# Kernel optimization log

Hardware: AMD Instinct MI355X
Metric: run time of the kernel (lower is better)

## Reference

```python
import jax, jax.numpy as jnp
import numpy as np

D_MODEL = 1024
NUM_HEADS = 16
HEAD_DIM = D_MODEL // NUM_HEADS


def setup_inputs() -> dict:
    key = jax.random.key(0)
    k_x, k_qw, k_qb, k_ow, k_ob = jax.random.split(key, 5)
    s = 1.0 / np.sqrt(D_MODEL)
    return {
        "x": jax.random.normal(k_x, (2, 2048, D_MODEL), dtype=jnp.float32),
        "qkv_w": jax.random.uniform(k_qw, (3 * D_MODEL, D_MODEL), jnp.float32, -s, s),
        "qkv_b": jax.random.uniform(k_qb, (3 * D_MODEL,), jnp.float32, -s, s),
        "out_w": jax.random.uniform(k_ow, (D_MODEL, D_MODEL), jnp.float32, -s, s),
        "out_b": jax.random.uniform(k_ob, (D_MODEL,), jnp.float32, -s, s),
    }


def reference(x, qkv_w, qkv_b, out_w, out_b):
    B, S, D = x.shape
    # fused QKV projection: [B,S,3D]
    qkv = jnp.einsum("bsd,ed->bse", x, qkv_w) + qkv_b
    # [B,S,H,3*hd] -> [B,H,S,3*hd]
    qkv = qkv.reshape(B, S, NUM_HEADS, 3 * HEAD_DIM).transpose(0, 2, 1, 3)
    q, k, v = jnp.split(qkv, 3, axis=-1)
    scale = 1.0 / jnp.sqrt(jnp.asarray(HEAD_DIM, x.dtype))
    scores = jnp.einsum("bhqd,bhkd->bhqk", q, k) * scale
    attn = jax.nn.softmax(scores, axis=-1)
    vals = jnp.einsum("bhqk,bhkd->bhqd", attn, v)
    vals = vals.transpose(0, 2, 1, 3).reshape(B, S, D)
    return jnp.einsum("bsd,ed->bse", vals, out_w) + out_b
```

## Files before the change

kernel.cpp:

```cpp
#include <hip/hip_runtime.h>
#include <stdint.h>


#define D_MODEL 1024
#define NUM_HEADS 16
#define HEAD_DIM 64
#define BATCH 2
#define SEQ 2048
#define M_TOT (BATCH * SEQ)
#define QKV_N (3 * D_MODEL)

typedef __attribute__((ext_vector_type(8))) short bf16x8;
typedef __attribute__((ext_vector_type(4))) short bf16x4;
typedef __attribute__((ext_vector_type(4))) float f32x4;
typedef __attribute__((ext_vector_type(4))) unsigned int u32x4;

__device__ __forceinline__ unsigned short f2bf(float f) {
    union { float f; unsigned int u; } v; v.f = f;
    unsigned int u = v.u;
    u += 0x7fffu + ((u >> 16) & 1u);
    return (unsigned short)(u >> 16);
}

__device__ __forceinline__ unsigned int exp2_bf16u(float x) {
    return (unsigned int)__builtin_fmaf(x, 128.0f, 16251.58f);
}

__device__ __forceinline__ unsigned int perm_pack(unsigned int hi, unsigned int lo) {
#if __has_builtin(__builtin_amdgcn_perm)
    return __builtin_amdgcn_perm(hi, lo, 0x05040100u);
#else
    return (lo & 0xFFFFu) | (hi << 16);
#endif
}

__device__ __forceinline__ void gld_lds16(const unsigned short* g,
                                          unsigned short* l) {
#if __has_builtin(__builtin_amdgcn_global_load_lds)
    __builtin_amdgcn_global_load_lds(
        (const __attribute__((address_space(1))) unsigned int*)g,
        (__attribute__((address_space(3))) unsigned int*)l, 16, 0, 0);
#else
    *(u32x4*)(l + (threadIdx.x & 63) * 8) = *(const u32x4*)g;
#endif
}

__global__ __launch_bounds__(256) void cvt_all(const float* __restrict__ x,
                                               const float* __restrict__ qw,
                                               const float* __restrict__ ow,
                                               unsigned short* __restrict__ xb,
                                               unsigned short* __restrict__ wqb,
                                               unsigned short* __restrict__ wob) {
    int i = blockIdx.x * 256 + threadIdx.x;
    const int N1 = M_TOT * D_MODEL / 8;
    const int N2 = N1 + QKV_N * D_MODEL / 8;
    const float* src; unsigned short* dst; int j;
    if (i < N1)      { src = x;  dst = xb;  j = i; }
    else if (i < N2) { src = qw; dst = wqb; j = i - N1; }
    else             { src = ow; dst = wob; j = i - N2; }
    const float4* s = (const float4*)src;
    float4 a = s[2 * j], b = s[2 * j + 1];
    u32x4 o;
    o.x = (unsigned int)f2bf(a.x) | ((unsigned int)f2bf(a.y) << 16);
    o.y = (unsigned int)f2bf(a.z) | ((unsigned int)f2bf(a.w) << 16);
    o.z = (unsigned int)f2bf(b.x) | ((unsigned int)f2bf(b.y) << 16);
    o.w = (unsigned int)f2bf(b.z) | ((unsigned int)f2bf(b.w) << 16);
    *(u32x4*)(dst + 8 * (size_t)j) = o;
}

__device__ __forceinline__ void gemm_tile(const unsigned short* __restrict__ A,
                                          const unsigned short* __restrict__ Bw,
                                          int K, int m0, int n0,
                                          unsigned short* As, unsigned short* Bs,
                                          f32x4 acc[4][4]) {
    const int tid = threadIdx.x;
    const int lane = tid & 63;
    const int wave = tid >> 6;
    const int wm = (wave >> 1) * 64;
    const int wn = (wave & 1) * 64;
    const int quad = lane >> 4;
    const int l16 = lane & 15;
    const int lrow = lane >> 3;
    const int sw = (lane & 7) ^ (lrow & 7);
    const int l7 = l16 & 7;

#pragma unroll
    for (int mt = 0; mt < 4; mt++)
#pragma unroll
        for (int nt = 0; nt < 4; nt++) acc[mt][nt] = (f32x4)0.0f;

    for (int kt = 0; kt < K; kt += 64) {
#pragma unroll
        for (int i = 0; i < 4; ++i) {
            int R = wave * 32 + i * 8;
            int grow = R + lrow;
            gld_lds16(A + (size_t)(m0 + grow) * K + kt + sw * 8, As + R * 64);
            gld_lds16(Bw + (size_t)(n0 + grow) * K + kt + sw * 8, Bs + R * 64);
        }
        __syncthreads();
#pragma unroll
        for (int ks = 0; ks < 2; ++ks) {
            int cxl = ((ks * 4 + quad) ^ l7) * 8;
            bf16x8 af[4], bf[4];
#pragma unroll
            for (int mt = 0; mt < 4; mt++)
                af[mt] = *(const bf16x8*)(As + (wm + mt * 16 + l16) * 64 + cxl);
#pragma unroll
            for (int nt = 0; nt < 4; nt++)
                bf[nt] = *(const bf16x8*)(Bs + (wn + nt * 16 + l16) * 64 + cxl);
#pragma unroll
            for (int mt = 0; mt < 4; mt++)
#pragma unroll
                for (int nt = 0; nt < 4; nt++)
                    acc[mt][nt] = __builtin_amdgcn_mfma_f32_16x16x32_bf16(
                        af[mt], bf[nt], acc[mt][nt], 0, 0, 0);
        }
        __syncthreads();
    }
}

__global__ __launch_bounds__(256) void gemm_qkv(const unsigned short* __restrict__ xb,
                                                const unsigned short* __restrict__ wb,
                                                const float* __restrict__ bias,
                                                unsigned short* __restrict__ qb,
                                                unsigned short* __restrict__ kb,
                                                unsigned short* __restrict__ vtb) {
    __shared__ __align__(16) unsigned short As[128 * 64];
    __shared__ __align__(16) unsigned short Bs[128 * 64];
    f32x4 acc[4][4];
    const int m0 = blockIdx.y * 128, n0 = blockIdx.x * 128;
    gemm_tile(xb, wb, D_MODEL, m0, n0, As, Bs, acc);

    const int tid = threadIdx.x;
    const int lane = tid & 63, wave = tid >> 6;
    const int wm = (wave >> 1) * 64, wn = (wave & 1) * 64;
    const int quad = lane >> 4, l16 = lane & 15;
    const float QSCALE = 0.18033688011112042f;

    const int s64 = (n0 + wn) >> 6;
    const int h = s64 / 3;
    const int sec = s64 - h * 3;
    const int bh = (m0 >> 11) * NUM_HEADS + h;
    const int sbase = (m0 + wm) & 2047;

    unsigned short* sm = ((wave & 2) ? Bs : As) + (wave & 1) * 4096;

    if (sec < 2) {
        const float scl = (sec == 0) ? QSCALE : 1.0f;
#pragma unroll
        for (int nt = 0; nt < 4; nt++) {
            int c = nt * 16 + l16;
            float bia = bias[n0 + wn + c];
#pragma unroll
            for (int mt = 0; mt < 4; mt++)
#pragma unroll
                for (int r = 0; r < 4; r++) {
                    int row = mt * 16 + quad * 4 + r;
                    sm[row * 64 + ((((c >> 3) ^ (row & 7)) << 3) | (c & 7))] =
                        f2bf((acc[mt][nt][r] + bia) * scl);
                }
        }
        unsigned short* dstb = (sec == 0) ? qb : kb;
#pragma unroll
        for (int p = 0; p < 8; p++) {
            int row = p * 8 + (lane >> 3);
            int g = lane & 7;
            u32x4 ch = *(const u32x4*)(sm + row * 64 + ((g ^ (row & 7)) << 3));
            *(u32x4*)(dstb + ((size_t)bh * SEQ + sbase + row) * 64 + g * 8) = ch;
        }
    } else {
#pragma unroll
        for (int nt = 0; nt < 4; nt++) {
            int d = nt * 16 + l16;
            float bia = bias[n0 + wn + d];
#pragma unroll
            for (int mt = 0; mt < 4; mt++) {
                int c = mt * 16 + quad * 4;
                unsigned short t4[4];
#pragma unroll
                for (int r = 0; r < 4; r++) t4[r] = f2bf(acc[mt][nt][r] + bia);
                *(uint64_t*)(sm + d * 64 +
                             ((((c >> 3) ^ (d & 7)) << 3) | (c & 7))) =
                    *(const uint64_t*)t4;
            }
        }
#pragma unroll
        for (int p = 0; p < 8; p++) {
            int row = p * 8 + (lane >> 3);
            int g = lane & 7;
            u32x4 ch = *(const u32x4*)(sm + row * 64 + ((g ^ (row & 7)) << 3));
            *(u32x4*)(vtb + ((size_t)bh * 64 + row) * SEQ + sbase + g * 8) = ch;
        }
    }
}

__global__ __launch_bounds__(256) void attn(const unsigned short* __restrict__ qb,
                                            const unsigned short* __restrict__ kb,
                                            const unsigned short* __restrict__ vtb,
                                            unsigned short* __restrict__ vals) {
    __shared__ __align__(16) unsigned short Ks[2][2][64 * 64];
    __shared__ __align__(16) unsigned short VTs[2][2][64 * 64];

    const int tid = threadIdx.x;
    const int lane = tid & 63, wave = tid >> 6;
    const int quad = lane >> 4, l16 = lane & 15;
    const int l7 = l16 & 7;
    const int bh = blockIdx.x;
    const int q0 = blockIdx.y * 128;
    const unsigned short* qh = qb + (size_t)bh * SEQ * 64;
    const unsigned short* kh = kb + (size_t)bh * SEQ * 64;
    const unsigned short* vth = vtb + (size_t)bh * 64 * SEQ;
    const int wrow = wave * 32;

    bf16x8 aq[2][2];
#pragma unroll
    for (int nq = 0; nq < 2; nq++)
#pragma unroll
        for (int ks = 0; ks < 2; ++ks)
            aq[nq][ks] = *(const bf16x8*)(
                qh + (size_t)(q0 + wrow + nq * 16 + l16) * 64 + ks * 32 + quad * 8);

    const int lrow = lane >> 3;
    const int sw = (lane & 7) ^ (lrow & 7);

    int cxl0 = ((0 * 4 + quad) ^ l7) * 8;
    int cxl1 = ((1 * 4 + quad) ^ l7) * 8;

    auto stage = [&](int t, int b) {
        int kt = t * 128;
#pragma unroll
        for (int h = 0; h < 2; ++h) {
            int kth = kt + h * 64;
#pragma unroll
            for (int i = 0; i < 2; ++i) {
                int R = wave * 16 + i * 8;
                int row = R + lrow;
                int krow = (row & 0x23) | ((row & 0x0C) << 1) | ((row & 0x10) >> 2);
                gld_lds16(kh + (size_t)(kth + krow) * 64 + sw * 8,
                          &Ks[b][h][R * 64]);
                gld_lds16(vth + (size_t)row * SEQ + kth + sw * 8,
                          &VTs[b][h][R * 64]);
            }
        }
    };

    stage(0, 0);
    __syncthreads();

    f32x4 oacc[2][4];
    f32x4 lsum[2];
#pragma unroll
    for (int mt = 0; mt < 2; mt++) {
        lsum[mt] = (f32x4)0.0f;
#pragma unroll
        for (int nt = 0; nt < 4; nt++) oacc[mt][nt] = (f32x4)0.0f;
    }

    bf16x8 ones8;
#pragma unroll
    for (int j = 0; j < 8; j++) ones8[j] = (short)0x3F80;

    const int NR = SEQ / 128;
    for (int t = 0; t < NR; ++t) {
        const int cur = t & 1;
        if (t + 1 < NR) stage(t + 1, cur ^ 1);

#pragma unroll
        for (int hf = 0; hf < 2; ++hf) {
            const unsigned short* Kc = Ks[cur][hf];
            const unsigned short* Vc = VTs[cur][hf];

            f32x4 sacc[4][2];
#pragma unroll
            for (int mk = 0; mk < 4; mk++)
#pragma unroll
                for (int nq = 0; nq < 2; nq++) sacc[mk][nq] = (f32x4)0.0f;
#pragma unroll
            for (int ks = 0; ks < 2; ++ks) {
                int cxl = ks ? cxl1 : cxl0;
                bf16x8 bk[4];
#pragma unroll
                for (int mk = 0; mk < 4; mk++)
                    bk[mk] = *(const bf16x8*)(Kc + (mk * 16 + l16) * 64 + cxl);
#pragma unroll
                for (int mk = 0; mk < 4; mk++)
#pragma unroll
                    for (int nq = 0; nq < 2; nq++)
                        sacc[mk][nq] = __builtin_amdgcn_mfma_f32_16x16x32_bf16(
                            bk[mk], aq[nq][ks], sacc[mk][nq], 0, 0, 0);
            }

            bf16x4 pf[4][2];
#pragma unroll
            for (int mk = 0; mk < 4; mk++)
#pragma unroll
                for (int nq = 0; nq < 2; nq++) {
                    unsigned int u0 = exp2_bf16u(sacc[mk][nq][0]);
                    unsigned int u1 = exp2_bf16u(sacc[mk][nq][1]);
                    unsigned int u2 = exp2_bf16u(sacc[mk][nq][2]);
                    unsigned int u3 = exp2_bf16u(sacc[mk][nq][3]);
                    union { unsigned int u[2]; bf16x4 b; } cv;
                    cv.u[0] = perm_pack(u1, u0);
                    cv.u[1] = perm_pack(u3, u2);
                    pf[mk][nq] = cv.b;
                }

#pragma unroll
            for (int w = 0; w < 2; ++w) {
                bf16x8 ap0 = __builtin_shufflevector(
                    pf[2 * w][0], pf[2 * w + 1][0], 0, 1, 2, 3, 4, 5, 6, 7);
                bf16x8 ap1 = __builtin_shufflevector(
                    pf[2 * w][1], pf[2 * w + 1][1], 0, 1, 2, 3, 4, 5, 6, 7);
                int cxl = w ? cxl1 : cxl0;
#pragma unroll
                for (int nt = 0; nt < 4; nt++) {
                    bf16x8 bv = *(const bf16x8*)(Vc + (nt * 16 + l16) * 64 + cxl);
                    oacc[0][nt] = __builtin_amdgcn_mfma_f32_16x16x32_bf16(
                        ap0, bv, oacc[0][nt], 0, 0, 0);
                    oacc[1][nt] = __builtin_amdgcn_mfma_f32_16x16x32_bf16(
                        ap1, bv, oacc[1][nt], 0, 0, 0);
                }
                lsum[0] = __builtin_amdgcn_mfma_f32_16x16x32_bf16(
                    ap0, ones8, lsum[0], 0, 0, 0);
                lsum[1] = __builtin_amdgcn_mfma_f32_16x16x32_bf16(
                    ap1, ones8, lsum[1], 0, 0, 0);
            }
        }
        __syncthreads();
    }

    const int b = bh >> 4, h = bh & 15;
#pragma unroll
    for (int mt = 0; mt < 2; mt++) {
        f32x4 inv;
#pragma unroll
        for (int r = 0; r < 4; r++) inv[r] = 1.0f / lsum[mt][r];
#pragma unroll
        for (int nt = 0; nt < 4; nt++) {
            int d = nt * 16 + l16;
#pragma unroll
            for (int r = 0; r < 4; r++) {
                int row = wrow + mt * 16 + quad * 4 + r;
                float v = oacc[mt][nt][r] * inv[r];
                vals[((size_t)(b * SEQ + q0 + row)) * D_MODEL + h * 64 + d] =
                    f2bf(v);
            }
        }
    }
}

__global__ __launch_bounds__(256) void gemm_out(const unsigned short* __restrict__ vb,
                                                const unsigned short* __restrict__ wb,
                                                const float* __restrict__ bias,
                                                float* __restrict__ out) {
    __shared__ __align__(16) unsigned short As[128 * 64];
    __shared__ __align__(16) unsigned short Bs[64 * 64];
    const int tid = threadIdx.x;
    const int lane = tid & 63, wave = tid >> 6;
    const int wm = (wave >> 1) * 64, wn = (wave & 1) * 32;
    const int quad = lane >> 4, l16 = lane & 15;
    const int lrow = lane >> 3;
    const int sw = (lane & 7) ^ (lrow & 7);
    const int l7 = l16 & 7;
    const int m0 = blockIdx.y * 128, n0 = blockIdx.x * 64;

    f32x4 acc[4][2];
#pragma unroll
    for (int mt = 0; mt < 4; mt++)
#pragma unroll
        for (int nt = 0; nt < 2; nt++) acc[mt][nt] = (f32x4)0.0f;

    for (int kt = 0; kt < D_MODEL; kt += 64) {
#pragma unroll
        for (int i = 0; i < 4; ++i) {
            int R = wave * 32 + i * 8;
            gld_lds16(vb + (size_t)(m0 + R + lrow) * D_MODEL + kt + sw * 8,
                      As + R * 64);
        }
#pragma unroll
        for (int i = 0; i < 2; ++i) {
            int R = wave * 16 + i * 8;
            gld_lds16(wb + (size_t)(n0 + R + lrow) * D_MODEL + kt + sw * 8,
                      Bs + R * 64);
        }
        __syncthreads();
#pragma unroll
        for (int ks = 0; ks < 2; ++ks) {
            int cxl = ((ks * 4 + quad) ^ l7) * 8;
            bf16x8 af[4], bf[2];
#pragma unroll
            for (int mt = 0; mt < 4; mt++)
                af[mt] = *(const bf16x8*)(As + (wm + mt * 16 + l16) * 64 + cxl);
#pragma unroll
            for (int nt = 0; nt < 2; nt++)
                bf[nt] = *(const bf16x8*)(Bs + (wn + nt * 16 + l16) * 64 + cxl);
#pragma unroll
            for (int mt = 0; mt < 4; mt++)
#pragma unroll
                for (int nt = 0; nt < 2; nt++)
                    acc[mt][nt] = __builtin_amdgcn_mfma_f32_16x16x32_bf16(
                        af[mt], bf[nt], acc[mt][nt], 0, 0, 0);
        }
        __syncthreads();
    }

#pragma unroll
    for (int mt = 0; mt < 4; mt++)
#pragma unroll
        for (int nt = 0; nt < 2; nt++) {
            int n = n0 + wn + nt * 16 + l16;
            float bia = bias[n];
#pragma unroll
            for (int r = 0; r < 4; r++) {
                int m = m0 + wm + mt * 16 + quad * 4 + r;
                out[(size_t)m * D_MODEL + n] = acc[mt][nt][r] + bia;
            }
        }
}

extern "C" void kernel_launch(void* const* d_in, const int* in_sizes, int n_in,
                              void* d_out, int out_size, void* d_ws, size_t ws_size,
                              hipStream_t stream) {
    const float* x = (const float*)d_in[0];
    const float* qkv_w = (const float*)d_in[1];
    const float* qkv_b = (const float*)d_in[2];
    const float* out_w = (const float*)d_in[3];
    const float* out_b = (const float*)d_in[4];
    float* out = (float*)d_out;

    char* ws = (char*)d_ws;
    size_t off = 0;
    auto carve = [&](size_t bytes) -> void* {
        void* p = ws + off;
        off += (bytes + 255) & ~(size_t)255;
        return p;
    };
    unsigned short* xb  = (unsigned short*)carve((size_t)M_TOT * D_MODEL * 2);
    unsigned short* wqb = (unsigned short*)carve((size_t)QKV_N * D_MODEL * 2);
    unsigned short* wob = (unsigned short*)carve((size_t)D_MODEL * D_MODEL * 2);
    unsigned short* qbuf = (unsigned short*)carve((size_t)M_TOT * D_MODEL * 2);
    unsigned short* kbuf = (unsigned short*)carve((size_t)M_TOT * D_MODEL * 2);
    unsigned short* vtb  = (unsigned short*)carve((size_t)M_TOT * D_MODEL * 2);
    unsigned short* vals = xb;

    const int NCHUNK = (M_TOT + QKV_N + D_MODEL) * D_MODEL / 8;
    cvt_all<<<NCHUNK / 256, 256, 0, stream>>>(x, qkv_w, out_w, xb, wqb, wob);

    gemm_qkv<<<dim3(QKV_N / 128, M_TOT / 128), 256, 0, stream>>>(
        xb, wqb, qkv_b, qbuf, kbuf, vtb);

    attn<<<dim3(BATCH * NUM_HEADS, SEQ / 128), 256, 0, stream>>>(
        qbuf, kbuf, vtb, vals);

    gemm_out<<<dim3(D_MODEL / 64, M_TOT / 128), 256, 0, stream>>>(
        vals, wob, out_b, out);
}
```

Baseline: 179.6 us.

## Double-buffer LDS tiles in QKV and output GEMMs to overlap loads with MFMA

Both projection GEMMs get two LDS buffers per operand. The next K-tile is issued with global-to-LDS loads into the alternate buffer while MFMAs consume the current one, which is meant to hide global-load latency behind compute. LDS use per block doubles, which may lower occupancy. Whether the async loads actually overlap depends on how gld_lds16 waits are placed relative to the remaining __syncthreads in the loop.

```diff
diff --git a/kernel.cpp b/kernel.cpp
--- a/kernel.cpp
+++ b/kernel.cpp
@@ -71,7 +71,8 @@
 __device__ __forceinline__ void gemm_tile(const unsigned short* __restrict__ A,
                                           const unsigned short* __restrict__ Bw,
                                           int K, int m0, int n0,
-                                          unsigned short* As, unsigned short* Bs,
+                                          unsigned short (*As)[128 * 64],
+                                          unsigned short (*Bs)[128 * 64],
                                           f32x4 acc[4][4]) {
     const int tid = threadIdx.x;
     const int lane = tid & 63;
@@ -89,25 +90,33 @@
 #pragma unroll
         for (int nt = 0; nt < 4; nt++) acc[mt][nt] = (f32x4)0.0f;
 
-    for (int kt = 0; kt < K; kt += 64) {
+    auto stage = [&](int kt, int b) {
 #pragma unroll
         for (int i = 0; i < 4; ++i) {
             int R = wave * 32 + i * 8;
             int grow = R + lrow;
-            gld_lds16(A + (size_t)(m0 + grow) * K + kt + sw * 8, As + R * 64);
-            gld_lds16(Bw + (size_t)(n0 + grow) * K + kt + sw * 8, Bs + R * 64);
-        }
-        __syncthreads();
+            gld_lds16(A + (size_t)(m0 + grow) * K + kt + sw * 8, As[b] + R * 64);
+            gld_lds16(Bw + (size_t)(n0 + grow) * K + kt + sw * 8, Bs[b] + R * 64);
+        }
+    };
+
+    stage(0, 0);
+    __syncthreads();
+
+    const int NT = K / 64;
+    for (int t = 0; t < NT; ++t) {
+        const int cur = t & 1;
+        if (t + 1 < NT) stage((t + 1) * 64, cur ^ 1);
 #pragma unroll
         for (int ks = 0; ks < 2; ++ks) {
             int cxl = ((ks * 4 + quad) ^ l7) * 8;
             bf16x8 af[4], bf[4];
 #pragma unroll
             for (int mt = 0; mt < 4; mt++)
-                af[mt] = *(const bf16x8*)(As + (wm + mt * 16 + l16) * 64 + cxl);
+                af[mt] = *(const bf16x8*)(As[cur] + (wm + mt * 16 + l16) * 64 + cxl);
 #pragma unroll
             for (int nt = 0; nt < 4; nt++)
-                bf[nt] = *(const bf16x8*)(Bs + (wn + nt * 16 + l16) * 64 + cxl);
+                bf[nt] = *(const bf16x8*)(Bs[cur] + (wn + nt * 16 + l16) * 64 + cxl);
 #pragma unroll
             for (int mt = 0; mt < 4; mt++)
 #pragma unroll
@@ -125,8 +134,8 @@
                                                 unsigned short* __restrict__ qb,
                                                 unsigned short* __restrict__ kb,
                                                 unsigned short* __restrict__ vtb) {
-    __shared__ __align__(16) unsigned short As[128 * 64];
-    __shared__ __align__(16) unsigned short Bs[128 * 64];
+    __shared__ __align__(16) unsigned short As[2][128 * 64];
+    __shared__ __align__(16) unsigned short Bs[2][128 * 64];
     f32x4 acc[4][4];
     const int m0 = blockIdx.y * 128, n0 = blockIdx.x * 128;
     gemm_tile(xb, wb, D_MODEL, m0, n0, As, Bs, acc);
@@ -143,7 +152,7 @@
     const int bh = (m0 >> 11) * NUM_HEADS + h;
     const int sbase = (m0 + wm) & 2047;
 
-    unsigned short* sm = ((wave & 2) ? Bs : As) + (wave & 1) * 4096;
+    unsigned short* sm = ((wave & 2) ? Bs[0] : As[0]) + (wave & 1) * 4096;
 
     if (sec < 2) {
         const float scl = (sec == 0) ? QSCALE : 1.0f;
@@ -353,8 +362,8 @@
                                                 const unsigned short* __restrict__ wb,
                                                 const float* __restrict__ bias,
                                                 float* __restrict__ out) {
-    __shared__ __align__(16) unsigned short As[128 * 64];
-    __shared__ __align__(16) unsigned short Bs[64 * 64];
+    __shared__ __align__(16) unsigned short As[2][128 * 64];
+    __shared__ __align__(16) unsigned short Bs[2][64 * 64];
     const int tid = threadIdx.x;
     const int lane = tid & 63, wave = tid >> 6;
     const int wm = (wave >> 1) * 64, wn = (wave & 1) * 32;
@@ -370,30 +379,38 @@
 #pragma unroll
         for (int nt = 0; nt < 2; nt++) acc[mt][nt] = (f32x4)0.0f;
 
-    for (int kt = 0; kt < D_MODEL; kt += 64) {
+    auto stage = [&](int kt, int b) {
 #pragma unroll
         for (int i = 0; i < 4; ++i) {
             int R = wave * 32 + i * 8;
             gld_lds16(vb + (size_t)(m0 + R + lrow) * D_MODEL + kt + sw * 8,
-                      As + R * 64);
+                      As[b] + R * 64);
         }
 #pragma unroll
         for (int i = 0; i < 2; ++i) {
             int R = wave * 16 + i * 8;
             gld_lds16(wb + (size_t)(n0 + R + lrow) * D_MODEL + kt + sw * 8,
-                      Bs + R * 64);
-        }
-        __syncthreads();
+                      Bs[b] + R * 64);
+        }
+    };
+
+    stage(0, 0);
+    __syncthreads();
+
+    const int NT = D_MODEL / 64;
+    for (int t = 0; t < NT; ++t) {
+        const int cur = t & 1;
+        if (t + 1 < NT) stage((t + 1) * 64, cur ^ 1);
 #pragma unroll
         for (int ks = 0; ks < 2; ++ks) {
             int cxl = ((ks * 4 + quad) ^ l7) * 8;
             bf16x8 af[4], bf[2];
 #pragma unroll
             for (int mt = 0; mt < 4; mt++)
-                af[mt] = *(const bf16x8*)(As + (wm + mt * 16 + l16) * 64 + cxl);
+                af[mt] = *(const bf16x8*)(As[cur] + (wm + mt * 16 + l16) * 64 + cxl);
 #pragma unroll
             for (int nt = 0; nt < 2; nt++)
-                bf[nt] = *(const bf16x8*)(Bs + (wn + nt * 16 + l16) * 64 + cxl);
+                bf[nt] = *(const bf16x8*)(Bs[cur] + (wn + nt * 16 + l16) * 64 + cxl);
 #pragma unroll
             for (int mt = 0; mt < 4; mt++)
 #pragma unroll
```

Measured after the change: 184.6 us. +2.8%, slower.
